# Kernel tuning notes

Hardware: AMD Instinct MI355X
Metric: run time of the kernel (lower is better)

The kernel has to match this reference:

```python
import jax, jax.numpy as jnp
import numpy as np

N_NODES = 50000
N_EDGES = 600000
N_GRAPHS = 2048
EMB = 128
N_LAYERS = 3
ATOM_FEATS, ATOM_VOCAB = 9, 100
BOND_FEATS, BOND_VOCAB, BOND_DIM = 3, 8, 3


def setup_inputs() -> dict:
    key = jax.random.key(0)
    ks = jax.random.split(key, 10)
    x = jax.random.randint(ks[0], (N_NODES, ATOM_FEATS), 0, ATOM_VOCAB)
    edge_index = jax.random.randint(ks[1], (2, N_EDGES), 0, N_NODES)
    edge_attr = jax.random.randint(ks[2], (N_EDGES, BOND_FEATS), 0, BOND_VOCAB)
    batch = jnp.sort(jax.random.randint(ks[3], (N_NODES,), 0, N_GRAPHS))
    s = 1.0 / np.sqrt(EMB).astype(np.float32)
    atom_emb = jax.random.normal(ks[4], (ATOM_FEATS, ATOM_VOCAB, EMB), jnp.float32) * 0.1
    bond_emb = jax.random.normal(ks[5], (N_LAYERS, BOND_FEATS, BOND_VOCAB, BOND_DIM), jnp.float32) * 0.1
    W = jax.random.normal(ks[6], (N_LAYERS, BOND_DIM, EMB, EMB), jnp.float32) * s
    b = jnp.zeros((N_LAYERS, BOND_DIM, EMB), jnp.float32)
    fc1_w = jax.random.normal(ks[7], (EMB, EMB), jnp.float32) * s
    fc1_b = jnp.zeros((EMB,), jnp.float32)
    fc2_w = jax.random.normal(ks[8], (EMB, 1), jnp.float32) * s
    fc2_b = jnp.zeros((1,), jnp.float32)
    return dict(x=x, edge_index=edge_index, edge_attr=edge_attr, batch=batch,
                atom_emb=atom_emb, bond_emb=bond_emb, W=W, b=b,
                fc1_w=fc1_w, fc1_b=fc1_b, fc2_w=fc2_w, fc2_b=fc2_b)


def reference(x, edge_index, edge_attr, batch, atom_emb, bond_emb, W, b,
              fc1_w, fc1_b, fc2_w, fc2_b):
    src, dst = edge_index[0], edge_index[1]
    n = x.shape[0]
    # AtomEncoder: sum of per-column embedding lookups -> [N, EMB]
    h = atom_emb[0][x[:, 0]]
    for c in range(1, ATOM_FEATS):
        h = h + atom_emb[c][x[:, c]]
    for layer in range(N_LAYERS):
        # BondEncoder: [E, BOND_DIM] edge weights (one scalar channel per conv)
        ew = bond_emb[layer, 0][edge_attr[:, 0]]
        for c in range(1, BOND_FEATS):
            ew = ew + bond_emb[layer, c][edge_attr[:, c]]
        # Three parallel GCNConv(normalize=False): linear, gather src, edge-weight, scatter-add to dst
        msg = jnp.zeros((edge_index.shape[1], EMB), h.dtype)
        for k in range(BOND_DIM):
            xw = h @ W[layer, k]              # [N, EMB]
            msg = msg + ew[:, k:k + 1] * xw[src]   # [E, EMB]
        agg = jax.ops.segment_sum(msg, dst, num_segments=n)
        hn = agg + jnp.sum(b[layer], axis=0)  # sum of the three conv biases
        if layer < N_LAYERS - 1:
            hn = jax.nn.relu(hn)              # dropout is identity at eval
        h = hn + h                            # residual
    # global_mean_pool
    sums = jax.ops.segment_sum(h, batch, num_segments=N_GRAPHS)
    counts = jax.ops.segment_sum(jnp.ones((n,), h.dtype), batch, num_segments=N_GRAPHS)
    hg = sums / jnp.maximum(counts, 1.0)[:, None]
    return (hg @ fc1_w + fc1_b) @ fc2_w + fc2_b   # [N_GRAPHS, 1]
```

## Files before the change

kernel.cpp:

```cpp
#include <hip/hip_runtime.h>

#define N_NODES 50000
#define N_EDGES 600000
#define N_GRAPHS 2048
#define EMB 128
#define TDIM 384
#define TS_LD 392
#define HN (N_NODES * EMB)
#define SCAN_NB ((N_NODES + 255) / 256)
#define DEG_STRIDE 32

#define PRE_ATOM_NB 8334
#define PRE_HIST_NB 1563
#define PRE_WCONV_NB 384
#define PRE_GB_NB 131

typedef __attribute__((ext_vector_type(8))) short bf16x8;
typedef __attribute__((ext_vector_type(4))) float f32x4;
#define MFMA_BF16(a, b, c) __builtin_amdgcn_mfma_f32_16x16x32_bf16(a, b, c, 0, 0, 0)

#define AS1 __attribute__((address_space(1)))
#define AS3 __attribute__((address_space(3)))
__device__ inline void gl_lds16(const void* g, void* l) {
  __builtin_amdgcn_global_load_lds((const AS1 void*)g, (AS3 void*)l, 16, 0, 0);
}

__device__ inline unsigned short f2bf(float f) {
  unsigned int u = __float_as_uint(f);
  u += 0x7fffu + ((u >> 16) & 1u);
  return (unsigned short)(u >> 16);
}
__device__ inline float bf2f(unsigned short b) {
  return __uint_as_float(((unsigned int)b) << 16);
}
__device__ inline bf16x8 pack8(float4 lo, float4 hi) {
  bf16x8 r;
  r[0] = (short)f2bf(lo.x); r[1] = (short)f2bf(lo.y);
  r[2] = (short)f2bf(lo.z); r[3] = (short)f2bf(lo.w);
  r[4] = (short)f2bf(hi.x); r[5] = (short)f2bf(hi.y);
  r[6] = (short)f2bf(hi.z); r[7] = (short)f2bf(hi.w);
  return r;
}

__global__ __launch_bounds__(384) void k_pre(const int* __restrict__ x,
                                             const float* __restrict__ atom_emb,
                                             unsigned short* __restrict__ h_bf,
                                             const int* __restrict__ ei,
                                             int* __restrict__ degP,
                                             int* __restrict__ rank,
                                             const float* __restrict__ W,
                                             unsigned short* __restrict__ wt,
                                             const int* __restrict__ batch,
                                             int* __restrict__ gs) {
  __shared__ float sb[6 * 1280];
  int blk = blockIdx.x;
  if (blk < PRE_ATOM_NB) {
    const int wv = threadIdx.x >> 6;
    const int lane = threadIdx.x & 63;
    int n = blk * 6 + wv;
    if (n < N_NODES) {
      const int nu = __builtin_amdgcn_readfirstlane(n);
      const int* xr = x + nu * 9;
      int ix[9];
#pragma unroll
      for (int c = 0; c < 9; ++c) ix[c] = xr[c];
      float* wbase = sb + wv * 1280;
      const int half = lane >> 5;
      const int sub16 = lane & 31;
#pragma unroll
      for (int j = 0; j < 4; ++j) {
        int c = 2 * j + half;
        const float* g = atom_emb + (size_t)(c * 100 + ix[c]) * EMB + sub16 * 4;
        gl_lds16(g, wbase + j * 256);
      }
      {
        const float* g = atom_emb + (size_t)(8 * 100 + ix[8]) * EMB + sub16 * 4;
        gl_lds16(g, wbase + 1024);
      }
      asm volatile("s_waitcnt vmcnt(0)" ::: "memory");
      float2 acc = {0.f, 0.f};
#pragma unroll
      for (int c = 0; c < 9; ++c) {
        float2 v = *(const float2*)(wbase + c * 128 + lane * 2);
        acc.x += v.x; acc.y += v.y;
      }
      *(ushort2*)(h_bf + (size_t)nu * EMB + lane * 2) = ushort2{f2bf(acc.x), f2bf(acc.y)};
    }
    return;
  }
  blk -= PRE_ATOM_NB;
  if (blk < PRE_HIST_NB) {
    int e = blk * 384 + threadIdx.x;
    if (e < N_EDGES) {
      int d = ei[N_EDGES + e];
      rank[e] = atomicAdd(&degP[(size_t)d * DEG_STRIDE], 1);
    }
    return;
  }
  blk -= PRE_HIST_NB;
  if (blk < PRE_WCONV_NB) {
    int layer = blk >> 7, c = blk & 127, k = threadIdx.x;
    float v = W[(((layer * 3 + (k >> 7)) * 128) + (k & 127)) * 128 + c];
    wt[(size_t)blk * 384 + k] = f2bf(v);
    return;
  }
  blk -= PRE_WCONV_NB;
  {
    int i = blk * 384 + threadIdx.x;
    if (i < N_NODES) {
      int b = batch[i];
      int bp = (i == 0) ? -1 : batch[i - 1];
      for (int g = bp + 1; g <= b; ++g) gs[g] = i;
      if (i == N_NODES - 1) {
        for (int g = b + 1; g <= N_GRAPHS; ++g) gs[g] = N_NODES;
      }
    }
  }
}

__global__ __launch_bounds__(256) void k_scan_a(const int* __restrict__ degP,
                                                int* __restrict__ row_start,
                                                int* __restrict__ partials) {
  __shared__ int s[256];
  const int tid = threadIdx.x;
  const int i = blockIdx.x * 256 + tid;
  int v = (i < N_NODES) ? degP[(size_t)i * DEG_STRIDE] : 0;
  s[tid] = v;
  __syncthreads();
  for (int off = 1; off < 256; off <<= 1) {
    int t = (tid >= off) ? s[tid - off] : 0;
    __syncthreads();
    s[tid] += t;
    __syncthreads();
  }
  if (i < N_NODES) row_start[i] = s[tid] - v;
  if (tid == 255) partials[blockIdx.x] = s[255];
}

__global__ __launch_bounds__(256) void k_scan_b(int* __restrict__ partials,
                                                int* __restrict__ row_start) {
  __shared__ int s[256];
  const int tid = threadIdx.x;
  int v = (tid < SCAN_NB) ? partials[tid] : 0;
  s[tid] = v;
  __syncthreads();
  for (int off = 1; off < 256; off <<= 1) {
    int t = (tid >= off) ? s[tid - off] : 0;
    __syncthreads();
    s[tid] += t;
    __syncthreads();
  }
  if (tid < SCAN_NB) partials[tid] = s[tid] - v;
  if (tid == 255) row_start[N_NODES] = s[255];
}

__global__ __launch_bounds__(256) void k_scan_c(int* __restrict__ row_start,
                                                const int* __restrict__ partials) {
  const int i = blockIdx.x * 256 + threadIdx.x;
  if (i < N_NODES) row_start[i] += partials[blockIdx.x];
}

__global__ __launch_bounds__(256) void k_scatter(const int* __restrict__ ei,
                                                 const int* __restrict__ ea,
                                                 const int* __restrict__ rank,
                                                 const int* __restrict__ row_start,
                                                 int2* __restrict__ sorted_se) {
  int e = blockIdx.x * 256 + threadIdx.x;
  if (e >= N_EDGES) return;
  int src = ei[e], dst = ei[N_EDGES + e];
  int pos = row_start[dst] + rank[e];
  int eap = ea[e * 3 + 0] | (ea[e * 3 + 1] << 3) | (ea[e * 3 + 2] << 6);
  sorted_se[pos] = int2{src, eap};
}

__global__ __launch_bounds__(256) void k_agg(const int2* __restrict__ sorted_se,
                                             const int* __restrict__ row_start,
                                             const float* __restrict__ bl,
                                             const unsigned short* __restrict__ h_bf,
                                             unsigned short* __restrict__ t_bf) {
  __shared__ float4 combo[512];
  for (int c = threadIdx.x; c < 512; c += 256) {
    int a0 = c & 7, a1 = (c >> 3) & 7, a2 = (c >> 6) & 7;
    combo[c] = float4{bl[a0 * 3 + 0] + bl[24 + a1 * 3 + 0] + bl[48 + a2 * 3 + 0],
                      bl[a0 * 3 + 1] + bl[24 + a1 * 3 + 1] + bl[48 + a2 * 3 + 1],
                      bl[a0 * 3 + 2] + bl[24 + a1 * 3 + 2] + bl[48 + a2 * 3 + 2], 0.f};
  }
  __syncthreads();
  const int node = blockIdx.x * 16 + (threadIdx.x >> 4);
  const int sub = threadIdx.x & 15;
  const int beg = row_start[node], end = row_start[node + 1];
  float4 l0 = {0.f, 0.f, 0.f, 0.f}, h0 = l0;
  float4 l1 = l0, h1 = l0;
  float4 l2 = l0, h2 = l0;
  int e = beg;
  const int full_end = beg + ((end - beg) & ~7);
  for (; e < full_end; e += 8) {
    int2 se[8];
#pragma unroll
    for (int j = 0; j < 8; ++j) se[j] = sorted_se[e + j];
    bf16x8 u[8];
#pragma unroll
    for (int j = 0; j < 8; ++j)
      u[j] = *(const bf16x8*)(h_bf + (size_t)se[j].x * EMB + sub * 8);
#pragma unroll
    for (int j = 0; j < 8; ++j) {
      float4 w = combo[se[j].y];
      float4 vlo = {bf2f((unsigned short)u[j][0]), bf2f((unsigned short)u[j][1]),
                    bf2f((unsigned short)u[j][2]), bf2f((unsigned short)u[j][3])};
      float4 vhi = {bf2f((unsigned short)u[j][4]), bf2f((unsigned short)u[j][5]),
                    bf2f((unsigned short)u[j][6]), bf2f((unsigned short)u[j][7])};
      l0 += vlo * w.x; h0 += vhi * w.x;
      l1 += vlo * w.y; h1 += vhi * w.y;
      l2 += vlo * w.z; h2 += vhi * w.z;
    }
  }
  if (e < end) {
    int2 se[8];
#pragma unroll
    for (int j = 0; j < 8; ++j) {
      int idx = e + j;
      se[j] = sorted_se[idx < end ? idx : end - 1];
    }
    bf16x8 u[8];
#pragma unroll
    for (int j = 0; j < 8; ++j)
      u[j] = *(const bf16x8*)(h_bf + (size_t)se[j].x * EMB + sub * 8);
#pragma unroll
    for (int j = 0; j < 8; ++j) {
      float4 w = (e + j < end) ? combo[se[j].y] : float4{0.f, 0.f, 0.f, 0.f};
      float4 vlo = {bf2f((unsigned short)u[j][0]), bf2f((unsigned short)u[j][1]),
                    bf2f((unsigned short)u[j][2]), bf2f((unsigned short)u[j][3])};
      float4 vhi = {bf2f((unsigned short)u[j][4]), bf2f((unsigned short)u[j][5]),
                    bf2f((unsigned short)u[j][6]), bf2f((unsigned short)u[j][7])};
      l0 += vlo * w.x; h0 += vhi * w.x;
      l1 += vlo * w.y; h1 += vhi * w.y;
      l2 += vlo * w.z; h2 += vhi * w.z;
    }
  }
  size_t base = (size_t)node * TDIM + sub * 8;
  *(bf16x8*)(t_bf + base)       = pack8(l0, h0);
  *(bf16x8*)(t_bf + base + 128) = pack8(l1, h1);
  *(bf16x8*)(t_bf + base + 256) = pack8(l2, h2);
}

__global__ __launch_bounds__(512) void k_gemm(const unsigned short* __restrict__ t_bf,
                                              const unsigned short* __restrict__ wt,
                                              const float* __restrict__ bl,
                                              const unsigned short* __restrict__ h_in_bf,
                                              unsigned short* __restrict__ h_out_bf,
                                              int do_relu) {
  __shared__ unsigned short ts[32 * TS_LD];
  const int nb = blockIdx.x * 32;
  for (int i = threadIdx.x; i < 32 * 48; i += 512) {
    int r = i / 48, cc = i % 48;
    bf16x8 v = {};
    int row = nb + r;
    if (row < N_NODES) v = *(const bf16x8*)(t_bf + (size_t)row * TDIM + cc * 8);
    *(bf16x8*)(ts + r * TS_LD + cc * 8) = v;
  }
  __syncthreads();

  const int wv = threadIdx.x >> 6;
  const int lane = threadIdx.x & 63;
  const int m = lane & 15;
  const int kq = lane >> 4;
  const int c = wv * 16 + m;

  const unsigned short* pB = wt + (size_t)c * TDIM + kq * 8;
  bf16x8 B[12];
#pragma unroll
  for (int kc = 0; kc < 12; ++kc) B[kc] = *(const bf16x8*)(pB + kc * 32);

  const float bias = bl[c] + bl[128 + c] + bl[256 + c];

#pragma unroll
  for (int rt = 0; rt < 2; ++rt) {
    const unsigned short* pA = ts + (rt * 16 + m) * TS_LD + kq * 8;
    bf16x8 A[12];
#pragma unroll
    for (int kc = 0; kc < 12; ++kc) A[kc] = *(const bf16x8*)(pA + kc * 32);
    f32x4 acc = {0.f, 0.f, 0.f, 0.f};
#pragma unroll
    for (int kc = 0; kc < 12; ++kc) acc = MFMA_BF16(A[kc], B[kc], acc);
#pragma unroll
    for (int r = 0; r < 4; ++r) {
      int row = nb + rt * 16 + kq * 4 + r;
      if (row < N_NODES) {
        size_t idx = (size_t)row * EMB + c;
        float v = acc[r] + bias;
        if (do_relu) v = fmaxf(v, 0.f);
        float hn = bf2f(h_in_bf[idx]) + v;
        h_out_bf[idx] = f2bf(hn);
      }
    }
  }
}

__global__ __launch_bounds__(128) void k_head(const unsigned short* __restrict__ h_bf,
                                              const int* __restrict__ gs,
                                              const float* __restrict__ fc1_w,
                                              const float* __restrict__ fc1_b,
                                              const float* __restrict__ fc2_w,
                                              const float* __restrict__ fc2_b,
                                              float* __restrict__ out) {
  __shared__ float hg[EMB];
  __shared__ float red[EMB];
  int g = blockIdx.x, e = threadIdx.x;
  int ns = gs[g], ne = gs[g + 1];
  float acc = 0.f;
  for (int n = ns; n < ne; ++n) acc += bf2f(h_bf[(size_t)n * EMB + e]);
  float cnt = fmaxf((float)(ne - ns), 1.f);
  hg[e] = acc / cnt;
  __syncthreads();
  float a2 = fc1_b[e];
  for (int j = 0; j < EMB; ++j) a2 += hg[j] * fc1_w[j * EMB + e];
  red[e] = a2 * fc2_w[e];
  __syncthreads();
  for (int s = 64; s > 0; s >>= 1) {
    if (e < s) red[e] += red[e + s];
    __syncthreads();
  }
  if (e == 0) out[g] = red[0] + fc2_b[0];
}

extern "C" void kernel_launch(void* const* d_in, const int* in_sizes, int n_in,
                              void* d_out, int out_size, void* d_ws, size_t ws_size,
                              hipStream_t stream) {
  const int*   x        = (const int*)d_in[0];
  const int*   ei       = (const int*)d_in[1];
  const int*   ea       = (const int*)d_in[2];
  const int*   batch    = (const int*)d_in[3];
  const float* atom_emb = (const float*)d_in[4];
  const float* bond_emb = (const float*)d_in[5];
  const float* W        = (const float*)d_in[6];
  const float* b        = (const float*)d_in[7];
  const float* fc1_w    = (const float*)d_in[8];
  const float* fc1_b    = (const float*)d_in[9];
  const float* fc2_w    = (const float*)d_in[10];
  const float* fc2_b    = (const float*)d_in[11];
  float* out = (float*)d_out;

  char* p = (char*)d_ws;
  auto alloc = [&](size_t bytes) { char* r = p; p += (bytes + 255) & ~(size_t)255; return r; };
  unsigned short* h0_bf      = (unsigned short*)alloc((size_t)HN * 2);
  unsigned short* h1_bf      = (unsigned short*)alloc((size_t)HN * 2);
  unsigned short* t_bf       = (unsigned short*)alloc((size_t)N_NODES * TDIM * 2);
  unsigned short* wt         = (unsigned short*)alloc((size_t)3 * 128 * TDIM * 2);
  int*            gs         = (int*)alloc((size_t)(N_GRAPHS + 1) * 4);
  int*            degP       = (int*)alloc((size_t)N_NODES * DEG_STRIDE * 4);
  int*            rank       = (int*)alloc((size_t)N_EDGES * 4);
  int*            row_start  = (int*)alloc((size_t)(N_NODES + 1) * 4);
  int*            partials   = (int*)alloc(256 * 4);
  int2*           sorted_se  = (int2*)alloc((size_t)(N_EDGES + 8) * 8);

  hipMemsetAsync(degP, 0, (size_t)N_NODES * DEG_STRIDE * sizeof(int), stream);
  const int pre_blocks = PRE_ATOM_NB + PRE_HIST_NB + PRE_WCONV_NB + PRE_GB_NB;
  k_pre<<<pre_blocks, 384, 0, stream>>>(x, atom_emb, h0_bf, ei, degP, rank, W, wt, batch, gs);
  k_scan_a<<<SCAN_NB, 256, 0, stream>>>(degP, row_start, partials);
  k_scan_b<<<1, 256, 0, stream>>>(partials, row_start);
  k_scan_c<<<SCAN_NB, 256, 0, stream>>>(row_start, partials);
  k_scatter<<<(N_EDGES + 255) / 256, 256, 0, stream>>>(ei, ea, rank, row_start, sorted_se);

  unsigned short* hib = h0_bf;
  unsigned short* hob = h1_bf;
  const int gemm_blocks = (N_NODES + 31) / 32;
  for (int layer = 0; layer < 3; ++layer) {
    k_agg<<<N_NODES / 16, 256, 0, stream>>>(sorted_se, row_start, bond_emb + layer * 72,
                                            hib, t_bf);
    k_gemm<<<gemm_blocks, 512, 0, stream>>>(
        t_bf, wt + (size_t)layer * 128 * TDIM, b + layer * 3 * EMB,
        hib, hob, layer < 2 ? 1 : 0);
    unsigned short* tb = hib; hib = hob; hob = tb;
  }

  k_head<<<N_GRAPHS, 128, 0, stream>>>(hib, gs, fc1_w, fc1_b, fc2_w, fc2_b, out);
}
```

Before: 348.3 us.

## Bucket nodes by degree for aggregation and use packed FMA accumulation

Adds three small kernels that group nodes into degree buckets and build a permutation, so each aggregation block handles nodes with similar edge counts. This is meant to cut divergence and load imbalance among the 16-lane groups in a block. The inner loop also switches to packed two-wide float FMAs on bf16 pairs to reduce ALU instruction count. In exchange there are extra launches, an indirection through perm, and output writes scattered by the permuted node order.

```diff
diff --git a/kernel.cpp b/kernel.cpp
--- a/kernel.cpp
+++ b/kernel.cpp
@@ -9,6 +9,7 @@
 #define HN (N_NODES * EMB)
 #define SCAN_NB ((N_NODES + 255) / 256)
 #define DEG_STRIDE 32
+#define NBUCKET 6
 
 #define PRE_ATOM_NB 8334
 #define PRE_HIST_NB 1563
@@ -17,6 +18,7 @@
 
 typedef __attribute__((ext_vector_type(8))) short bf16x8;
 typedef __attribute__((ext_vector_type(4))) float f32x4;
+typedef __attribute__((ext_vector_type(2))) float f32x2;
 #define MFMA_BF16(a, b, c) __builtin_amdgcn_mfma_f32_16x16x32_bf16(a, b, c, 0, 0, 0)
 
 #define AS1 __attribute__((address_space(1)))
@@ -33,12 +35,22 @@
 __device__ inline float bf2f(unsigned short b) {
   return __uint_as_float(((unsigned int)b) << 16);
 }
-__device__ inline bf16x8 pack8(float4 lo, float4 hi) {
+
+__device__ inline f32x2 bfpair(unsigned int d) {
+  f32x2 r;
+  r.x = __uint_as_float(d << 16);
+  r.y = __uint_as_float(d & 0xffff0000u);
+  return r;
+}
+__device__ inline void pkfma(f32x2& a, f32x2 v, float w) {
+  a = __builtin_elementwise_fma(v, f32x2{w, w}, a);
+}
+__device__ inline bf16x8 pack8p(const f32x2* a) {
   bf16x8 r;
-  r[0] = (short)f2bf(lo.x); r[1] = (short)f2bf(lo.y);
-  r[2] = (short)f2bf(lo.z); r[3] = (short)f2bf(lo.w);
-  r[4] = (short)f2bf(hi.x); r[5] = (short)f2bf(hi.y);
-  r[6] = (short)f2bf(hi.z); r[7] = (short)f2bf(hi.w);
+  r[0] = (short)f2bf(a[0].x); r[1] = (short)f2bf(a[0].y);
+  r[2] = (short)f2bf(a[1].x); r[3] = (short)f2bf(a[1].y);
+  r[4] = (short)f2bf(a[2].x); r[5] = (short)f2bf(a[2].y);
+  r[6] = (short)f2bf(a[3].x); r[7] = (short)f2bf(a[3].y);
   return r;
 }
 
@@ -160,6 +172,49 @@
   if (i < N_NODES) row_start[i] += partials[blockIdx.x];
 }
 
+__global__ __launch_bounds__(256) void k_bucket_a(const int* __restrict__ row_start,
+                                                  int* __restrict__ nrank,
+                                                  int* __restrict__ bcntP,
+                                                  int* __restrict__ blk_base)
+{
+  __shared__ int cnt[8];
+  const int tid = threadIdx.x;
+  const int i = blockIdx.x * 256 + tid;
+  if (tid < 8) cnt[tid] = 0;
+  __syncthreads();
+  if (i < N_NODES) {
+    int deg = row_start[i + 1] - row_start[i];
+    int c = (deg + 7) >> 3;
+    if (c > NBUCKET - 1) c = NBUCKET - 1;
+    int rl = atomicAdd(&cnt[c], 1);
+    nrank[i] = c | (rl << 3);
+  }
+  __syncthreads();
+  if (tid < NBUCKET) {
+    int n = cnt[tid];
+    blk_base[blockIdx.x * 8 + tid] = n ? atomicAdd(&bcntP[tid * 32], n) : 0;
+  }
+}
+
+__global__ void k_bucket_b(const int* __restrict__ bcntP, int* __restrict__ bucket_base) {
+  if (threadIdx.x == 0 && blockIdx.x == 0) {
+    int s = 0;
+    for (int c = 0; c < NBUCKET; ++c) { bucket_base[c] = s; s += bcntP[c * 32]; }
+  }
+}
+
+__global__ __launch_bounds__(256) void k_bucket_c(const int* __restrict__ nrank,
+                                                  const int* __restrict__ bucket_base,
+                                                  const int* __restrict__ blk_base,
+                                                  int* __restrict__ perm) {
+  const int i = blockIdx.x * 256 + threadIdx.x;
+  if (i < N_NODES) {
+    int v = nrank[i];
+    int c = v & 7, rl = v >> 3;
+    perm[bucket_base[c] + blk_base[blockIdx.x * 8 + c] + rl] = i;
+  }
+}
+
 __global__ __launch_bounds__(256) void k_scatter(const int* __restrict__ ei,
                                                  const int* __restrict__ ea,
                                                  const int* __restrict__ rank,
@@ -175,6 +230,7 @@
 
 __global__ __launch_bounds__(256) void k_agg(const int2* __restrict__ sorted_se,
                                              const int* __restrict__ row_start,
+                                             const int* __restrict__ perm,
                                              const float* __restrict__ bl,
                                              const unsigned short* __restrict__ h_bf,
                                              unsigned short* __restrict__ t_bf) {
@@ -186,32 +242,28 @@
                       bl[a0 * 3 + 2] + bl[24 + a1 * 3 + 2] + bl[48 + a2 * 3 + 2], 0.f};
   }
   __syncthreads();
-  const int node = blockIdx.x * 16 + (threadIdx.x >> 4);
+  const int node = perm[blockIdx.x * 16 + (threadIdx.x >> 4)];
   const int sub = threadIdx.x & 15;
   const int beg = row_start[node], end = row_start[node + 1];
-  float4 l0 = {0.f, 0.f, 0.f, 0.f}, h0 = l0;
-  float4 l1 = l0, h1 = l0;
-  float4 l2 = l0, h2 = l0;
+  f32x2 a0[4] = {}, a1[4] = {}, a2[4] = {};
   int e = beg;
   const int full_end = beg + ((end - beg) & ~7);
   for (; e < full_end; e += 8) {
     int2 se[8];
 #pragma unroll
     for (int j = 0; j < 8; ++j) se[j] = sorted_se[e + j];
-    bf16x8 u[8];
+    uint4 u[8];
 #pragma unroll
     for (int j = 0; j < 8; ++j)
-      u[j] = *(const bf16x8*)(h_bf + (size_t)se[j].x * EMB + sub * 8);
+      u[j] = *(const uint4*)(h_bf + (size_t)se[j].x * EMB + sub * 8);
 #pragma unroll
     for (int j = 0; j < 8; ++j) {
       float4 w = combo[se[j].y];
-      float4 vlo = {bf2f((unsigned short)u[j][0]), bf2f((unsigned short)u[j][1]),
-                    bf2f((unsigned short)u[j][2]), bf2f((unsigned short)u[j][3])};
-      float4 vhi = {bf2f((unsigned short)u[j][4]), bf2f((unsigned short)u[j][5]),
-                    bf2f((unsigned short)u[j][6]), bf2f((unsigned short)u[j][7])};
-      l0 += vlo * w.x; h0 += vhi * w.x;
-      l1 += vlo * w.y; h1 += vhi * w.y;
-      l2 += vlo * w.z; h2 += vhi * w.z;
+      f32x2 v0 = bfpair(u[j].x), v1 = bfpair(u[j].y),
+            v2 = bfpair(u[j].z), v3 = bfpair(u[j].w);
+      pkfma(a0[0], v0, w.x); pkfma(a0[1], v1, w.x); pkfma(a0[2], v2, w.x); pkfma(a0[3], v3, w.x);
+      pkfma(a1[0], v0, w.y); pkfma(a1[1], v1, w.y); pkfma(a1[2], v2, w.y); pkfma(a1[3], v3, w.y);
+      pkfma(a2[0], v0, w.z); pkfma(a2[1], v1, w.z); pkfma(a2[2], v2, w.z); pkfma(a2[3], v3, w.z);
     }
   }
   if (e < end) {
@@ -221,26 +273,24 @@
       int idx = e + j;
       se[j] = sorted_se[idx < end ? idx : end - 1];
     }
-    bf16x8 u[8];
+    uint4 u[8];
 #pragma unroll
     for (int j = 0; j < 8; ++j)
-      u[j] = *(const bf16x8*)(h_bf + (size_t)se[j].x * EMB + sub * 8);
+      u[j] = *(const uint4*)(h_bf + (size_t)se[j].x * EMB + sub * 8);
 #pragma unroll
     for (int j = 0; j < 8; ++j) {
       float4 w = (e + j < end) ? combo[se[j].y] : float4{0.f, 0.f, 0.f, 0.f};
-      float4 vlo = {bf2f((unsigned short)u[j][0]), bf2f((unsigned short)u[j][1]),
-                    bf2f((unsigned short)u[j][2]), bf2f((unsigned short)u[j][3])};
-      float4 vhi = {bf2f((unsigned short)u[j][4]), bf2f((unsigned short)u[j][5]),
-                    bf2f((unsigned short)u[j][6]), bf2f((unsigned short)u[j][7])};
-      l0 += vlo * w.x; h0 += vhi * w.x;
-      l1 += vlo * w.y; h1 += vhi * w.y;
-      l2 += vlo * w.z; h2 += vhi * w.z;
+      f32x2 v0 = bfpair(u[j].x), v1 = bfpair(u[j].y),
+            v2 = bfpair(u[j].z), v3 = bfpair(u[j].w);
+      pkfma(a0[0], v0, w.x); pkfma(a0[1], v1, w.x); pkfma(a0[2], v2, w.x); pkfma(a0[3], v3, w.x);
+      pkfma(a1[0], v0, w.y); pkfma(a1[1], v1, w.y); pkfma(a1[2], v2, w.y); pkfma(a1[3], v3, w.y);
+      pkfma(a2[0], v0, w.z); pkfma(a2[1], v1, w.z); pkfma(a2[2], v2, w.z); pkfma(a2[3], v3, w.z);
     }
   }
   size_t base = (size_t)node * TDIM + sub * 8;
-  *(bf16x8*)(t_bf + base)       = pack8(l0, h0);
-  *(bf16x8*)(t_bf + base + 128) = pack8(l1, h1);
-  *(bf16x8*)(t_bf + base + 256) = pack8(l2, h2);
+  *(bf16x8*)(t_bf + base)       = pack8p(a0);
+  *(bf16x8*)(t_bf + base + 128) = pack8p(a1);
+  *(bf16x8*)(t_bf + base + 256) = pack8p(a2);
 }
 
 __global__ __launch_bounds__(512) void k_gemm(const unsigned short* __restrict__ t_bf,
@@ -351,22 +401,31 @@
   int*            rank       = (int*)alloc((size_t)N_EDGES * 4);
   int*            row_start  = (int*)alloc((size_t)(N_NODES + 1) * 4);
   int*            partials   = (int*)alloc(256 * 4);
+  int*            nrank      = (int*)alloc((size_t)N_NODES * 4);
+  int*            perm       = (int*)alloc((size_t)N_NODES * 4);
+  int*            bcntP      = (int*)alloc((size_t)NBUCKET * 32 * 4);
+  int*            blk_base   = (int*)alloc((size_t)SCAN_NB * 8 * 4);
+  int*            bucket_base= (int*)alloc(64);
   int2*           sorted_se  = (int2*)alloc((size_t)(N_EDGES + 8) * 8);
 
   hipMemsetAsync(degP, 0, (size_t)N_NODES * DEG_STRIDE * sizeof(int), stream);
+  hipMemsetAsync(bcntP, 0, (size_t)NBUCKET * 32 * sizeof(int), stream);
   const int pre_blocks = PRE_ATOM_NB + PRE_HIST_NB + PRE_WCONV_NB + PRE_GB_NB;
   k_pre<<<pre_blocks, 384, 0, stream>>>(x, atom_emb, h0_bf, ei, degP, rank, W, wt, batch, gs);
   k_scan_a<<<SCAN_NB, 256, 0, stream>>>(degP, row_start, partials);
   k_scan_b<<<1, 256, 0, stream>>>(partials, row_start);
   k_scan_c<<<SCAN_NB, 256, 0, stream>>>(row_start, partials);
+  k_bucket_a<<<SCAN_NB, 256, 0, stream>>>(row_start, nrank, bcntP, blk_base);
+  k_bucket_b<<<1, 64, 0, stream>>>(bcntP, bucket_base);
+  k_bucket_c<<<SCAN_NB, 256, 0, stream>>>(nrank, bucket_base, blk_base, perm);
   k_scatter<<<(N_EDGES + 255) / 256, 256, 0, stream>>>(ei, ea, rank, row_start, sorted_se);
 
   unsigned short* hib = h0_bf;
   unsigned short* hob = h1_bf;
   const int gemm_blocks = (N_NODES + 31) / 32;
   for (int layer = 0; layer < 3; ++layer) {
-    k_agg<<<N_NODES / 16, 256, 0, stream>>>(sorted_se, row_start, bond_emb + layer * 72,
-                                            hib, t_bf);
+    k_agg<<<N_NODES / 16, 256, 0, stream>>>(sorted_se, row_start, perm,
+                                            bond_emb + layer * 72, hib, t_bf);
     k_gemm<<<gemm_blocks, 512, 0, stream>>>(
         t_bf, wt + (size_t)layer * 128 * TDIM, b + layer * 3 * EMB,
         hib, hob, layer < 2 ? 1 : 0);
```

Result: slower. 356.4 us (+2.3%).
